# Performance work log

Measured on AMD Instinct MI355X. Metric: run time of the kernel, lower is better.

The kernel has to match this reference:

```python
import math
import jax, jax.numpy as jnp
import numpy as np

B, L, C, H = 8, 1024, 1024, 16
D = C // H  # head_dim = 64
MAX_SCALE_MUL = math.log(100.0)


def setup_inputs() -> dict:
    key = jax.random.key(0)
    ks = jax.random.split(key, 8)
    x = jax.random.normal(ks[0], (B, L, C), dtype=jnp.float32)
    # rotary frequencies: angle(l, j) = l * theta^(-2j/D), stored as (cos, sin)
    theta = 10000.0
    inv_freq = theta ** (-jnp.arange(0, D, 2, dtype=jnp.float32) / D)  # [D/2]
    ang = jnp.arange(L, dtype=jnp.float32)[:, None] * inv_freq[None, :]  # [L, D/2]
    freqs_cis = jnp.stack([jnp.cos(ang), jnp.sin(ang)], axis=-1)  # [L, D/2, 2]
    attn_bias = jnp.zeros((1, 1, L, L), dtype=jnp.float32)
    W_qkv = jax.random.normal(ks[1], (3 * C, C), dtype=jnp.float32) * (1.0 / math.sqrt(C))
    q_bias = jnp.zeros((C,), dtype=jnp.float32)
    v_bias = jnp.zeros((C,), dtype=jnp.float32)
    scale_mul_log = jnp.full((1, H, 1, 1), math.log(4.0), dtype=jnp.float32)
    W_proj = jax.random.normal(ks[2], (C, C), dtype=jnp.float32) * (1.0 / math.sqrt(C))
    b_proj = jnp.zeros((C,), dtype=jnp.float32)
    return {"x": x, "freqs_cis": freqs_cis, "attn_bias": attn_bias,
            "W_qkv": W_qkv, "q_bias": q_bias, "v_bias": v_bias,
            "scale_mul_log": scale_mul_log, "W_proj": W_proj, "b_proj": b_proj}


def _l2norm(t):
    # F.normalize(t, dim=-1): t / max(||t||_2, eps)
    n = jnp.sqrt(jnp.sum(t * t, axis=-1, keepdims=True))
    return t / jnp.maximum(n, 1e-12)


def _rope(t, fr):
    # t: [B,H,L,D]; fr: [L,D/2,2] (cos,sin). Complex mul on adjacent pairs.
    b, h, l, d = t.shape
    t2 = t.reshape(b, h, l, d // 2, 2)
    c = fr[None, None, :, :, 0]
    s = fr[None, None, :, :, 1]
    re = t2[..., 0] * c - t2[..., 1] * s
    im = t2[..., 0] * s + t2[..., 1] * c
    return jnp.stack([re, im], axis=-1).reshape(b, h, l, d)


def reference(x, freqs_cis, attn_bias, W_qkv, q_bias, v_bias, scale_mul_log, W_proj, b_proj):
    b, l, c = x.shape
    bias = jnp.concatenate([q_bias, jnp.zeros_like(q_bias), v_bias])  # [3C]
    qkv = (x @ W_qkv.T + bias).reshape(b, l, 3, H, D)
    # permute(2,0,3,1,4) -> q,k,v each [B,H,L,D]
    q = jnp.transpose(qkv[:, :, 0], (0, 2, 1, 3))
    k = jnp.transpose(qkv[:, :, 1], (0, 2, 1, 3))
    v = jnp.transpose(qkv[:, :, 2], (0, 2, 1, 3))
    # attn_l2_norm path: learned per-head scale, softmax scale = 1
    scale_mul = jnp.exp(jnp.minimum(scale_mul_log, MAX_SCALE_MUL))  # [1,H,1,1]
    q = _l2norm(q) * scale_mul
    k = _l2norm(k)
    q = _rope(q, freqs_cis)
    k = _rope(k, freqs_cis)
    scores = jnp.einsum('bhqd,bhkd->bhqk', q, k) * 1.0 + attn_bias
    attn = jax.nn.softmax(scores, axis=-1)
    out = jnp.einsum('bhqk,bhkd->bhqd', attn, v)
    out = jnp.transpose(out, (0, 2, 1, 3)).reshape(b, l, c)
    return out @ W_proj.T + b_proj
```

## Files before the change

kernel.cpp:

```cpp
#include <hip/hip_runtime.h>
#include <math.h>

#define PB 8
#define PL 1024
#define PC 1024
#define PH 16
#define PD 64
#define MAX_SCALE_MUL 4.605170185988092f
#define LOG2E 1.4426950408889634f

typedef __attribute__((ext_vector_type(8))) short s16x8;
typedef __attribute__((ext_vector_type(4))) float f32x4;

#define MFMA16(a, b, c) __builtin_amdgcn_mfma_f32_16x16x32_bf16(a, b, c, 0, 0, 0)

#if __has_builtin(__builtin_amdgcn_exp2f)
#define EXP2(x) __builtin_amdgcn_exp2f(x)
#else
#define EXP2(x) exp2f(x)
#endif

__device__ __forceinline__ unsigned short f2bf(float f) {
    unsigned u = __float_as_uint(f);
    unsigned r = (u + 0x7fffu + ((u >> 16) & 1u)) >> 16;
    return (unsigned short)r;
}

__device__ __forceinline__ unsigned pk2bf(float a, float b) {
#if __has_builtin(__builtin_amdgcn_cvt_pk_bf16_f32)
    typedef __attribute__((ext_vector_type(2))) __bf16 bf16x2_t;
    bf16x2_t r = __builtin_amdgcn_cvt_pk_bf16_f32(a, b);
    return __builtin_bit_cast(unsigned, r);
#else
    return (unsigned)f2bf(a) | ((unsigned)f2bf(b) << 16);
#endif
}

__device__ __forceinline__ void gl2lds16(const void* g, void* l) {
    __builtin_amdgcn_global_load_lds(
        (const __attribute__((address_space(1))) unsigned int*)g,
        (__attribute__((address_space(3))) unsigned int*)l, 16, 0, 0);
}

__global__ __launch_bounds__(256) void cast3f_kernel(
    const float* __restrict__ a, const float* __restrict__ b,
    const float* __restrict__ c, const float* __restrict__ bias,
    unsigned short* __restrict__ oa, unsigned short* __restrict__ ob,
    unsigned short* __restrict__ oc, int* __restrict__ flag)
{
    int blk = blockIdx.x;
    if (blk >= 12288) {
        int idx = (blk - 12288) * 256 + threadIdx.x;
        const float4* b4 = (const float4*)bias;
        bool nz = false;
#pragma unroll
        for (int i = 0; i < 4; i++) {
            float4 v = b4[idx * 4 + i];
            nz |= (v.x != 0.f) | (v.y != 0.f) | (v.z != 0.f) | (v.w != 0.f);
        }
        if (nz) atomicOr(flag, 1);
        return;
    }
    const float* src; unsigned short* dst; int base;
    if (blk < 8192)       { src = a; dst = oa; base = blk; }
    else if (blk < 11264) { src = b; dst = ob; base = blk - 8192; }
    else                  { src = c; dst = oc; base = blk - 11264; }
    int i = base * 256 + threadIdx.x;
    float4 v = ((const float4*)src)[i];
    ((uint2*)dst)[i] = make_uint2(pk2bf(v.x, v.y), pk2bf(v.z, v.w));
}

template<int VMODE>
__global__ __launch_bounds__(256) void gemm_qkv_lean(
    const unsigned short* __restrict__ Xh,
    const unsigned short* __restrict__ Wh,
    const float* __restrict__ qb, const float* __restrict__ vb,
    const float* __restrict__ freqs,
    unsigned short* __restrict__ Qh, unsigned short* __restrict__ Kh,
    unsigned short* __restrict__ Vt)
{
    __shared__ unsigned short As[128 * 64];
    __shared__ unsigned short Bs[128 * 64];
    const int tid  = threadIdx.x;
    const int wave = tid >> 6, lane = tid & 63;
    const int wm = wave & 1, wn = wave >> 1;
    const int quad = lane >> 4, rr = lane & 15;
    const int m0 = blockIdx.x * 128;
    const int n0 = (blockIdx.y + (VMODE ? 16 : 0)) * 128;

    f32x4 acc[4][4];
#pragma unroll
    for (int i = 0; i < 4; i++)
#pragma unroll
        for (int j = 0; j < 4; j++) acc[i][j] = (f32x4){0.f, 0.f, 0.f, 0.f};

    const int r8 = lane >> 3;
    const int c8 = lane & 7;
    const int g  = c8 ^ r8;
    const unsigned short* gA = Xh + (size_t)(m0 + wave * 32 + r8) * 1024 + g * 8;
    const unsigned short* gB = Wh + (size_t)(n0 + wave * 32 + r8) * 1024 + g * 8;
    unsigned short* lA = &As[(wave * 32) * 64];
    unsigned short* lB = &Bs[(wave * 32) * 64];

    const int swz8 = rr & 7;

    for (int k0 = 0; k0 < 16; k0++) {
#pragma unroll
        for (int t = 0; t < 4; t++) {
            gl2lds16(gA + (size_t)t * 8192, &lA[(t * 8) * 64]);
            gl2lds16(gB + (size_t)t * 8192, &lB[(t * 8) * 64]);
        }
        gA += 64; gB += 64;
        __syncthreads();

#pragma unroll
        for (int kk = 0; kk < 2; kk++) {
            const int coff = ((kk * 4 + quad) ^ swz8) * 8;
            s16x8 wf[4], xf[4];
#pragma unroll
            for (int i = 0; i < 4; i++)
                wf[i] = *(const s16x8*)&Bs[(wn * 64 + i * 16 + rr) * 64 + coff];
#pragma unroll
            for (int j = 0; j < 4; j++)
                xf[j] = *(const s16x8*)&As[(wm * 64 + j * 16 + rr) * 64 + coff];
            if constexpr (VMODE == 0) {
#pragma unroll
                for (int i = 0; i < 4; i++)
#pragma unroll
                    for (int j = 0; j < 4; j++)
                        acc[i][j] = MFMA16(wf[i], xf[j], acc[i][j]);
            } else {
#pragma unroll
                for (int i = 0; i < 4; i++)
#pragma unroll
                    for (int j = 0; j < 4; j++)
                        acc[i][j] = MFMA16(xf[j], wf[i], acc[i][j]);
            }
        }
        __syncthreads();
    }

    const int b   = m0 >> 10;
    const int h   = ((n0 & 1023) + wn * 64) >> 6;
    const int lb0 = (m0 & 1023) + wm * 64;

    if constexpr (VMODE) {
        unsigned short* basep = Vt + (size_t)(b * PH + h) * PD * PL;
#pragma unroll
        for (int i = 0; i < 4; i++) {
            const int d = i * 16 + rr;
            const float bv = vb[h * 64 + d];
#pragma unroll
            for (int j = 0; j < 4; j++) {
                const int l0 = lb0 + j * 16 + quad * 4;
                uint2 pk = make_uint2(pk2bf(acc[i][j][0] + bv, acc[i][j][1] + bv),
                                      pk2bf(acc[i][j][2] + bv, acc[i][j][3] + bv));
                *(uint2*)(basep + (size_t)d * PL + l0) = pk;
            }
        }
    } else {
        const int which = n0 >> 10;
        if (which == 0) {
            unsigned short* basep = Qh + (size_t)(b * PH + h) * PL * PD;
#pragma unroll
            for (int i = 0; i < 4; i++) {
                const int d0 = i * 16 + quad * 4;
                const float4 b4 = *(const float4*)(qb + h * 64 + d0);
#pragma unroll
                for (int j = 0; j < 4; j++) {
                    const int l = lb0 + j * 16 + rr;
                    uint2 pk = make_uint2(
                        pk2bf(acc[i][j][0] + b4.x, acc[i][j][1] + b4.y),
                        pk2bf(acc[i][j][2] + b4.z, acc[i][j][3] + b4.w));
                    *(uint2*)(basep + (size_t)l * PD + d0) = pk;
                }
            }
        } else {
            unsigned short* basep = Kh + (size_t)(b * PH + h) * PL * PD;
            const float2* fr2 = (const float2*)freqs;
#pragma unroll
            for (int j = 0; j < 4; j++) {
                float ss = 0.f;
#pragma unroll
                for (int i = 0; i < 4; i++)
                    ss = fmaf(acc[i][j][0], acc[i][j][0],
                         fmaf(acc[i][j][1], acc[i][j][1],
                         fmaf(acc[i][j][2], acc[i][j][2],
                         fmaf(acc[i][j][3], acc[i][j][3], ss))));
                ss += __shfl_xor(ss, 16);
                ss += __shfl_xor(ss, 32);
                const float scale = 1.0f / fmaxf(sqrtf(ss), 1e-12f);
                const int l = lb0 + j * 16 + rr;
#pragma unroll
                for (int i = 0; i < 4; i++) {
                    const int d0 = i * 16 + quad * 4;
                    const float2 cs0 = fr2[(size_t)l * 32 + (d0 >> 1)];
                    const float2 cs1 = fr2[(size_t)l * 32 + (d0 >> 1) + 1];
                    const float a0 = acc[i][j][0] * scale, a1 = acc[i][j][1] * scale;
                    const float a2 = acc[i][j][2] * scale, a3 = acc[i][j][3] * scale;
                    uint2 pk = make_uint2(
                        pk2bf(a0 * cs0.x - a1 * cs0.y, fmaf(a0, cs0.y, a1 * cs0.x)),
                        pk2bf(a2 * cs1.x - a3 * cs1.y, fmaf(a2, cs1.y, a3 * cs1.x)));
                    *(uint2*)(basep + (size_t)l * PD + d0) = pk;
                }
            }
        }
    }
}

__global__ __launch_bounds__(256, 3) void attn_mfma(
    const unsigned short* __restrict__ Qh, const unsigned short* __restrict__ Kh,
    const unsigned short* __restrict__ Vt, const float* __restrict__ bias,
    const float* __restrict__ sml, const int* __restrict__ biasflag,
    const float* __restrict__ freqs, unsigned short* __restrict__ O)
{
    __shared__ unsigned short Ks[2][64 * 64];
    __shared__ unsigned short Vs[2][64 * 64];
    __shared__ unsigned int   Ps[4][16 * 32];

    const int tid  = threadIdx.x;
    const int wave = tid >> 6, lane = tid & 63;
    const int quad = lane >> 4, rr = lane & 15;
    const int bh = blockIdx.x, q0 = blockIdx.y * 128;
    const int b = bh >> 4, h = bh & 15;
    const int hasbias = *biasflag;

    const float M = __expf(fminf(sml[h], MAX_SCALE_MUL)) * LOG2E;
    const f32x4 negM = (f32x4){-M, -M, -M, -M};

    const int sr = wave * 16 + (lane >> 3);
    const int sc = lane & 7;
    const int sg = sc ^ (sr & 7);
    const int swz8 = rr & 7;
    const int psw  = (rr & 7) << 2;

    const size_t kvbase = (size_t)bh * PL * PD;
    const float2* fr2 = (const float2*)freqs;

    auto stage = [&](int buf, int kb) {
        gl2lds16(Kh + kvbase + (size_t)(kb * 64 + sr) * PD + sg * 8,
                 &Ks[buf][(wave * 16) * 64]);
        gl2lds16(Kh + kvbase + (size_t)(kb * 64 + sr + 8) * PD + sg * 8,
                 &Ks[buf][(wave * 16 + 8) * 64]);
        gl2lds16(Vt + kvbase + (size_t)sr * PL + kb * 64 + sg * 8,
                 &Vs[buf][(wave * 16) * 64]);
        gl2lds16(Vt + kvbase + (size_t)(sr + 8) * PL + kb * 64 + sg * 8,
                 &Vs[buf][(wave * 16 + 8) * 64]);
    };

    stage(0, 0);

    s16x8 qB[2][2];
#pragma unroll
    for (int g = 0; g < 2; g++) {
        const int ql = q0 + g * 64 + wave * 16 + rr;
        const size_t qoff = ((size_t)bh * PL + ql) * PD;
        uint4 r0 = *(const uint4*)(Qh + qoff + quad * 8);
        uint4 r1 = *(const uint4*)(Qh + qoff + 32 + quad * 8);
        unsigned uu[8] = {r0.x, r0.y, r0.z, r0.w, r1.x, r1.y, r1.z, r1.w};
        float lo[8], hi[8];
        float ss = 0.f;
#pragma unroll
        for (int m = 0; m < 8; m++) {
            lo[m] = __uint_as_float(uu[m] << 16);
            hi[m] = __uint_as_float(uu[m] & 0xffff0000u);
            ss = fmaf(lo[m], lo[m], fmaf(hi[m], hi[m], ss));
        }
        ss += __shfl_xor(ss, 16);
        ss += __shfl_xor(ss, 32);
        const float scale = M / fmaxf(sqrtf(ss), 1e-12f);
        unsigned outw[8];
#pragma unroll
        for (int m = 0; m < 8; m++) {
            const int idx = (m >> 2) * 16 + quad * 4 + (m & 3);
            float2 cs = fr2[(size_t)ql * 32 + idx];
            float av = lo[m] * scale, bv = hi[m] * scale;
            float re = av * cs.x - bv * cs.y;
            float im = fmaf(av, cs.y, bv * cs.x);
            outw[m] = pk2bf(re, im);
        }
        uint4 w0 = make_uint4(outw[0], outw[1], outw[2], outw[3]);
        uint4 w1 = make_uint4(outw[4], outw[5], outw[6], outw[7]);
        qB[g][0] = __builtin_bit_cast(s16x8, w0);
        qB[g][1] = __builtin_bit_cast(s16x8, w1);
    }

    f32x4 accO[2][4];
#pragma unroll
    for (int g = 0; g < 2; g++)
#pragma unroll
        for (int jd = 0; jd < 4; jd++) accO[g][jd] = (f32x4){0.f, 0.f, 0.f, 0.f};
    float lsum[2] = {0.f, 0.f};

    __syncthreads();

    int cur = 0;
    for (int kb = 0; kb < 16; kb++) {
        if (kb < 15) stage(cur ^ 1, kb + 1);

        unsigned ps[2][4][2];
#pragma unroll
        for (int s = 0; s < 4; s++) {
            const s16x8 k0 = *(const s16x8*)&Ks[cur][(s * 16 + rr) * 64 + ((0 + quad) ^ swz8) * 8];
            const s16x8 k1 = *(const s16x8*)&Ks[cur][(s * 16 + rr) * 64 + ((4 + quad) ^ swz8) * 8];
#pragma unroll
            for (int g = 0; g < 2; g++) {
                __builtin_amdgcn_s_setprio(1);
                f32x4 z = MFMA16(k0, qB[g][0], negM);
                z = MFMA16(k1, qB[g][1], z);
                __builtin_amdgcn_s_setprio(0);
                if (hasbias) {
                    const float* brow = bias + (size_t)(q0 + g * 64 + wave * 16 + rr) * PL + kb * 64;
                    float4 bv = *(const float4*)(brow + s * 16 + quad * 4);
                    z[0] = fmaf(bv.x, LOG2E, z[0]);
                    z[1] = fmaf(bv.y, LOG2E, z[1]);
                    z[2] = fmaf(bv.z, LOG2E, z[2]);
                    z[3] = fmaf(bv.w, LOG2E, z[3]);
                }
                z[0] = EXP2(z[0]); z[1] = EXP2(z[1]);
                z[2] = EXP2(z[2]); z[3] = EXP2(z[3]);
                lsum[g] += (z[0] + z[1]) + (z[2] + z[3]);
                ps[g][s][0] = pk2bf(z[0], z[1]);
                ps[g][s][1] = pk2bf(z[2], z[3]);
            }
        }

        s16x8 pB[2][2];
#pragma unroll
        for (int g = 0; g < 2; g++) {
#pragma unroll
            for (int s = 0; s < 4; s++)
                *(uint2*)&Ps[wave][rr * 32 + ((s * 8 + quad * 2) ^ psw)] =
                    make_uint2(ps[g][s][0], ps[g][s][1]);
            pB[g][0] = *(const s16x8*)&Ps[wave][rr * 32 + ((quad * 4) ^ psw)];
            pB[g][1] = *(const s16x8*)&Ps[wave][rr * 32 + ((16 + quad * 4) ^ psw)];
        }
#pragma unroll
        for (int jd = 0; jd < 4; jd++) {
            const s16x8 v0 = *(const s16x8*)&Vs[cur][(jd * 16 + rr) * 64 + ((0 + quad) ^ swz8) * 8];
            const s16x8 v1 = *(const s16x8*)&Vs[cur][(jd * 16 + rr) * 64 + ((4 + quad) ^ swz8) * 8];
            __builtin_amdgcn_s_setprio(1);
#pragma unroll
            for (int g = 0; g < 2; g++) {
                accO[g][jd] = MFMA16(v0, pB[g][0], accO[g][jd]);
                accO[g][jd] = MFMA16(v1, pB[g][1], accO[g][jd]);
            }
            __builtin_amdgcn_s_setprio(0);
        }

        __syncthreads();
        cur ^= 1;
    }

    const int lr = lane >> 2, cch = lane & 3;
    const int pswl = (lr & 7) << 2;
#pragma unroll
    for (int g = 0; g < 2; g++) {
        float ls = lsum[g];
        ls += __shfl_xor(ls, 16);
        ls += __shfl_xor(ls, 32);
        float inv = 1.0f / ls;
#pragma unroll
        for (int jd = 0; jd < 4; jd++) {
            *(uint2*)&Ps[wave][rr * 32 + ((jd * 8 + quad * 2) ^ psw)] =
                make_uint2(pk2bf(accO[g][jd][0] * inv, accO[g][jd][1] * inv),
                           pk2bf(accO[g][jd][2] * inv, accO[g][jd][3] * inv));
        }
        uint4 w0 = *(const uint4*)&Ps[wave][lr * 32 + ((cch * 8) ^ pswl)];
        uint4 w1 = *(const uint4*)&Ps[wave][lr * 32 + ((cch * 8 + 4) ^ pswl)];
        size_t ob = ((size_t)(b * PL + q0 + g * 64 + wave * 16 + lr) * PC + h * PD);
        *(uint4*)(O + ob + cch * 16)     = w0;
        *(uint4*)(O + ob + cch * 16 + 8) = w1;
    }
}

__global__ __launch_bounds__(256) void gemm_proj_mfma(
    const unsigned short* __restrict__ Ah,
    const unsigned short* __restrict__ Wh,
    const float* __restrict__ bp, float* __restrict__ Out)
{
    __shared__ unsigned short As[128 * 64];
    __shared__ unsigned short Bs[128 * 64];
    const int tid  = threadIdx.x;
    const int wave = tid >> 6, lane = tid & 63;
    const int wm = wave & 1, wn = wave >> 1;
    const int quad = lane >> 4, rr = lane & 15;
    const int m0 = blockIdx.x * 128, n0 = blockIdx.y * 128;

    f32x4 acc[4][4];
#pragma unroll
    for (int i = 0; i < 4; i++)
#pragma unroll
        for (int j = 0; j < 4; j++) acc[i][j] = (f32x4){0.f, 0.f, 0.f, 0.f};

    const int r8 = lane >> 3;
    const int c8 = lane & 7;
    const int g  = c8 ^ r8;
    const unsigned short* gA = Ah + (size_t)(m0 + wave * 32 + r8) * 1024 + g * 8;
    const unsigned short* gB = Wh + (size_t)(n0 + wave * 32 + r8) * 1024 + g * 8;
    unsigned short* lA = &As[(wave * 32) * 64];
    unsigned short* lB = &Bs[(wave * 32) * 64];

    const int swz8 = rr & 7;

    for (int k0 = 0; k0 < 16; k0++) {
#pragma unroll
        for (int t = 0; t < 4; t++) {
            gl2lds16(gA + (size_t)t * 8192, &lA[(t * 8) * 64]);
            gl2lds16(gB + (size_t)t * 8192, &lB[(t * 8) * 64]);
        }
        gA += 64; gB += 64;
        __syncthreads();

#pragma unroll
        for (int kk = 0; kk < 2; kk++) {
            const int coff = ((kk * 4 + quad) ^ swz8) * 8;
            s16x8 wf[4], xf[4];
#pragma unroll
            for (int i = 0; i < 4; i++)
                wf[i] = *(const s16x8*)&Bs[(wn * 64 + i * 16 + rr) * 64 + coff];
#pragma unroll
            for (int j = 0; j < 4; j++)
                xf[j] = *(const s16x8*)&As[(wm * 64 + j * 16 + rr) * 64 + coff];
#pragma unroll
            for (int i = 0; i < 4; i++)
#pragma unroll
                for (int j = 0; j < 4; j++)
                    acc[i][j] = MFMA16(wf[i], xf[j], acc[i][j]);
        }
        __syncthreads();
    }

#pragma unroll
    for (int i = 0; i < 4; i++) {
        const int nn = n0 + wn * 64 + i * 16 + quad * 4;
        const float4 bb = *(const float4*)(bp + nn);
#pragma unroll
        for (int j = 0; j < 4; j++) {
            const int m = m0 + wm * 64 + j * 16 + rr;
            float4 o = make_float4(acc[i][j][0] + bb.x, acc[i][j][1] + bb.y,
                                   acc[i][j][2] + bb.z, acc[i][j][3] + bb.w);
            *(float4*)(Out + (size_t)m * 1024 + nn) = o;
        }
    }
}

extern "C" void kernel_launch(void* const* d_in, const int* in_sizes, int n_in,
                              void* d_out, int out_size, void* d_ws, size_t ws_size,
                              hipStream_t stream)
{
    const float* x         = (const float*)d_in[0];
    const float* freqs     = (const float*)d_in[1];
    const float* attn_bias = (const float*)d_in[2];
    const float* W_qkv     = (const float*)d_in[3];
    const float* q_bias    = (const float*)d_in[4];
    const float* v_bias    = (const float*)d_in[5];
    const float* sml       = (const float*)d_in[6];
    const float* W_proj    = (const float*)d_in[7];
    const float* b_proj    = (const float*)d_in[8];
    float* out = (float*)d_out;

    unsigned char* w = (unsigned char*)d_ws;
    const size_t MB = 1ull << 20;
    unsigned short* xh  = (unsigned short*)(w + 0);
    unsigned short* wqh = (unsigned short*)(w + 16 * MB);
    unsigned short* wph = (unsigned short*)(w + 22 * MB);
    unsigned short* Qh  = (unsigned short*)(w + 24 * MB);
    unsigned short* Kh  = (unsigned short*)(w + 40 * MB);
    unsigned short* Vt  = (unsigned short*)(w + 72 * MB);
    unsigned short* Oh  = (unsigned short*)(w + 88 * MB);
    int*            flg = (int*)(w + 104 * MB);

    hipMemsetAsync(flg, 0, sizeof(int), stream);
    cast3f_kernel<<<12544, 256, 0, stream>>>(x, W_qkv, W_proj, attn_bias,
                                             xh, wqh, wph, flg);
    gemm_qkv_lean<0><<<dim3(64, 16), 256, 0, stream>>>(
        xh, wqh, q_bias, v_bias, freqs, Qh, Kh, Vt);
    gemm_qkv_lean<1><<<dim3(64, 8), 256, 0, stream>>>(
        xh, wqh, q_bias, v_bias, freqs, Qh, Kh, Vt);
    attn_mfma<<<dim3(128, 8), 256, 0, stream>>>(Qh, Kh, Vt, attn_bias, sml, flg, freqs, Oh);
    gemm_proj_mfma<<<dim3(64, 8), 256, 0, stream>>>(Oh, wph, b_proj, out);
}
```

Baseline: 268.5 us.

## Load K/V fragments directly from global memory instead of LDS double-buffering

Removes the shared-memory double-buffered staging of K and V tiles and their block-wide barriers in the attention kernel. Each wave now reads its MFMA operand fragments straight from global memory, counting on L1/L2 to serve the reuse across waves. The grid is transposed so that the q-blocks of the same head are adjacent in launch order, which should improve cache sharing of K/V, and the occupancy hint in the launch bounds is dropped. This gives up explicit prefetch overlap and LDS reuse in exchange for less LDS, no barriers, and possibly higher occupancy.

New measurement: 318.9 us. 1.19x slower.

```diff
diff --git a/kernel.cpp b/kernel.cpp
--- a/kernel.cpp
+++ b/kernel.cpp
@@ -208,47 +208,29 @@
     }
 }
 
-__global__ __launch_bounds__(256, 3) void attn_mfma(
+__global__ __launch_bounds__(256) void attn_mfma(
     const unsigned short* __restrict__ Qh, const unsigned short* __restrict__ Kh,
     const unsigned short* __restrict__ Vt, const float* __restrict__ bias,
     const float* __restrict__ sml, const int* __restrict__ biasflag,
     const float* __restrict__ freqs, unsigned short* __restrict__ O)
 {
-    __shared__ unsigned short Ks[2][64 * 64];
-    __shared__ unsigned short Vs[2][64 * 64];
-    __shared__ unsigned int   Ps[4][16 * 32];
+    __shared__ unsigned int Ps[4][16 * 32];
 
     const int tid  = threadIdx.x;
     const int wave = tid >> 6, lane = tid & 63;
     const int quad = lane >> 4, rr = lane & 15;
-    const int bh = blockIdx.x, q0 = blockIdx.y * 128;
+    const int q0 = blockIdx.x * 128;
+    const int bh = blockIdx.y;
     const int b = bh >> 4, h = bh & 15;
     const int hasbias = *biasflag;
 
     const float M = __expf(fminf(sml[h], MAX_SCALE_MUL)) * LOG2E;
     const f32x4 negM = (f32x4){-M, -M, -M, -M};
 
-    const int sr = wave * 16 + (lane >> 3);
-    const int sc = lane & 7;
-    const int sg = sc ^ (sr & 7);
-    const int swz8 = rr & 7;
-    const int psw  = (rr & 7) << 2;
+    const int psw = (rr & 7) << 2;
 
     const size_t kvbase = (size_t)bh * PL * PD;
     const float2* fr2 = (const float2*)freqs;
-
-    auto stage = [&](int buf, int kb) {
-        gl2lds16(Kh + kvbase + (size_t)(kb * 64 + sr) * PD + sg * 8,
-                 &Ks[buf][(wave * 16) * 64]);
-        gl2lds16(Kh + kvbase + (size_t)(kb * 64 + sr + 8) * PD + sg * 8,
-                 &Ks[buf][(wave * 16 + 8) * 64]);
-        gl2lds16(Vt + kvbase + (size_t)sr * PL + kb * 64 + sg * 8,
-                 &Vs[buf][(wave * 16) * 64]);
-        gl2lds16(Vt + kvbase + (size_t)(sr + 8) * PL + kb * 64 + sg * 8,
-                 &Vs[buf][(wave * 16 + 8) * 64]);
-    };
-
-    stage(0, 0);
 
     s16x8 qB[2][2];
 #pragma unroll
@@ -292,17 +274,14 @@
         for (int jd = 0; jd < 4; jd++) accO[g][jd] = (f32x4){0.f, 0.f, 0.f, 0.f};
     float lsum[2] = {0.f, 0.f};
 
-    __syncthreads();
-
-    int cur = 0;
     for (int kb = 0; kb < 16; kb++) {
-        if (kb < 15) stage(cur ^ 1, kb + 1);
-
         unsigned ps[2][4][2];
 #pragma unroll
         for (int s = 0; s < 4; s++) {
-            const s16x8 k0 = *(const s16x8*)&Ks[cur][(s * 16 + rr) * 64 + ((0 + quad) ^ swz8) * 8];
-            const s16x8 k1 = *(const s16x8*)&Ks[cur][(s * 16 + rr) * 64 + ((4 + quad) ^ swz8) * 8];
+            const unsigned short* kp =
+                Kh + kvbase + (size_t)(kb * 64 + s * 16 + rr) * PD + quad * 8;
+            const s16x8 k0 = *(const s16x8*)kp;
+            const s16x8 k1 = *(const s16x8*)(kp + 32);
 #pragma unroll
             for (int g = 0; g < 2; g++) {
                 __builtin_amdgcn_s_setprio(1);
@@ -337,8 +316,10 @@
         }
 #pragma unroll
         for (int jd = 0; jd < 4; jd++) {
-            const s16x8 v0 = *(const s16x8*)&Vs[cur][(jd * 16 + rr) * 64 + ((0 + quad) ^ swz8) * 8];
-            const s16x8 v1 = *(const s16x8*)&Vs[cur][(jd * 16 + rr) * 64 + ((4 + quad) ^ swz8) * 8];
+            const unsigned short* vp =
+                Vt + kvbase + (size_t)(jd * 16 + rr) * PL + kb * 64 + quad * 8;
+            const s16x8 v0 = *(const s16x8*)vp;
+            const s16x8 v1 = *(const s16x8*)(vp + 32);
             __builtin_amdgcn_s_setprio(1);
 #pragma unroll
             for (int g = 0; g < 2; g++) {
@@ -347,9 +328,6 @@
             }
             __builtin_amdgcn_s_setprio(0);
         }
-
-        __syncthreads();
-        cur ^= 1;
     }
 
     const int lr = lane >> 2, cch = lane & 3;
@@ -478,6 +456,6 @@
         xh, wqh, q_bias, v_bias, freqs, Qh, Kh, Vt);
     gemm_qkv_lean<1><<<dim3(64, 8), 256, 0, stream>>>(
         xh, wqh, q_bias, v_bias, freqs, Qh, Kh, Vt);
-    attn_mfma<<<dim3(128, 8), 256, 0, stream>>>(Qh, Kh, Vt, attn_bias, sml, flg, freqs, Oh);
+    attn_mfma<<<dim3(8, 128), 256, 0, stream>>>(Qh, Kh, Vt, attn_bias, sml, flg, freqs, Oh);
     gemm_proj_mfma<<<dim3(64, 8), 256, 0, stream>>>(Oh, wph, b_proj, out);
 }
```
